# Kernel optimization log

Hardware: AMD Instinct MI355X
Metric: run time of the kernel (lower is better)

The kernel has to match this reference:

```python
import jax, jax.numpy as jnp
import numpy as np

R = 8            # ring rank
N = 4            # num cores
D_IN = 2048
D_OUT = 2048
LIN = [512, 512, 512, 512]   # local input dims (additive split)
LOUT = [512, 512, 512, 512]  # local output dims (additive split)


def setup_inputs() -> dict:
    key = jax.random.key(0)
    ks = jax.random.split(key, 6)
    inp = {"inputs": jax.random.normal(ks[0], (4, 1024, D_IN), dtype=jnp.float32)}
    for i in range(N):
        lf = LOUT[i] * LIN[i]
        std = np.sqrt(2.0 / (R + lf)).astype(np.float32)
        inp[f"core{i}"] = jax.random.normal(ks[1 + i], (R, lf, R), dtype=jnp.float32) * std
    inp["bias"] = jnp.zeros((D_OUT,), dtype=jnp.float32)
    return inp


def reference(inputs, core0, core1, core2, core3, bias):
    cores = [core0, core1, core2, core3]
    batch_shape = inputs.shape[:-1]
    x = inputs.reshape(-1, D_IN)                      # [B, D_IN]
    B = x.shape[0]

    # split input additively across cores
    offs = np.cumsum([0] + LIN)
    xs = [x[:, offs[i]:offs[i + 1]] for i in range(N)]  # each [B, d_in_i]
    Gs = [cores[i].reshape(R, LOUT[i], LIN[i], R) for i in range(N)]

    # environment messages: S_i[b,r,s] = sum_{o,x} G_i[r,o,x,s] * x_i[b,x]
    S = [jnp.einsum('roxs,bx->brs', Gs[i], xs[i]) for i in range(N)]

    eye = jnp.broadcast_to(jnp.eye(R, dtype=x.dtype), (B, R, R))
    # prefix P_i = S_0 ... S_{i-1}, suffix Q_i = S_{i+1} ... S_{N-1}
    P = [eye]
    for i in range(1, N):
        P.append(jnp.matmul(P[-1], S[i - 1]))
    Q = [eye]
    for i in range(N - 2, -1, -1):
        Q.append(jnp.matmul(S[i + 1], Q[-1]))
    Q = Q[::-1]

    outs = []
    for i in range(N):
        # Env_i[b,r,s] = sum_p Q_i[b,s,p] P_i[b,p,r]  (trace closure of the ring)
        env = jnp.einsum('bsp,bpr->brs', Q[i], P[i])
        # M_i[b,r,o,s] = sum_x G_i[r,o,x,s] x_i[b,x]
        M = jnp.einsum('roxs,bx->bros', Gs[i], xs[i])
        outs.append(jnp.einsum('brs,bros->bo', env, M))
    out = jnp.concatenate(outs, axis=-1) + bias       # [B, D_OUT]
    return out.reshape(batch_shape + (D_OUT,))
```

## Files before the change

kernel.cpp:

```cpp
#include <hip/hip_runtime.h>

#define B_TOT   4096
#define D_IN    2048
#define D_OUT   2048
#define NCHUNK  4
#define LIN     512
#define LOUT    512
#define RK      8
#define KXS     4096
#define CORE_R_STRIDE 2097152
#define CORE_O_STRIDE 4096

#define WS_XT    0
#define WS_GHAT  8388608
#define WS_S     (8388608 + 131072)
#define WS_ENVT  (8388608 + 131072 + 1048576)

typedef __attribute__((ext_vector_type(8))) __bf16 bf16x8;
typedef __attribute__((ext_vector_type(4))) float f32x4;
typedef __attribute__((ext_vector_type(4))) unsigned int u32x4;

__global__ __launch_bounds__(256) void k_transpose(const float* __restrict__ x,
                                                   float* __restrict__ xT) {
    __shared__ float tile[32][33];
    int b0 = blockIdx.x * 32;
    int c0 = blockIdx.y * 32;
    int tx = threadIdx.x;
    int ty = threadIdx.y;
#pragma unroll
    for (int j = 0; j < 4; ++j)
        tile[ty + j * 8][tx] = x[(size_t)(b0 + ty + j * 8) * D_IN + c0 + tx];
    __syncthreads();
#pragma unroll
    for (int j = 0; j < 4; ++j)
        xT[(size_t)(c0 + ty + j * 8) * B_TOT + b0 + tx] = tile[tx][ty + j * 8];
}

__global__ __launch_bounds__(256) void k_reduce_g(const float* __restrict__ g0,
                                                  const float* __restrict__ g1,
                                                  const float* __restrict__ g2,
                                                  const float* __restrict__ g3,
                                                  float* __restrict__ ghat) {
    int i = blockIdx.z;
    int r = blockIdx.y;
    int xs = blockIdx.x * 256 + threadIdx.x;
    const float* G = (i == 0) ? g0 : (i == 1) ? g1 : (i == 2) ? g2 : g3;
    const float* base = G + (size_t)r * CORE_R_STRIDE + xs;
    float acc = 0.f;
#pragma unroll 8
    for (int o = 0; o < LOUT; ++o) acc += base[(size_t)o * CORE_O_STRIDE];
    ghat[(size_t)i * 32768 + r * 4096 + xs] = acc;
}

__global__ __launch_bounds__(256) void k_s(const float* __restrict__ x,
                                           const float* __restrict__ ghat,
                                           float* __restrict__ S) {
    int i = blockIdx.y;
    int tid = threadIdx.x;
    int rs = tid & 63;
    int b = blockIdx.x * 4 + (tid >> 6);
    int r = rs >> 3, s = rs & 7;
    const float* gh = ghat + (size_t)i * 32768 + r * 4096 + s;
    const float* xr = x + (size_t)b * D_IN + i * LIN;
    float acc = 0.f;
#pragma unroll 8
    for (int xi = 0; xi < LIN; ++xi) acc = fmaf(gh[xi * 8], xr[xi], acc);
    S[(size_t)i * (B_TOT * 64) + b * 64 + rs] = acc;
}

__device__ __forceinline__ float mm8(float A, float B, int lane) {
    float c = 0.f;
#pragma unroll
    for (int p = 0; p < 8; ++p) {
        float a = __shfl(A, (lane & 56) | p, 64);
        float b = __shfl(B, (p << 3) | (lane & 7), 64);
        c = fmaf(a, b, c);
    }
    return c;
}
__device__ __forceinline__ float tr8(float E, int lane) {
    return __shfl(E, ((lane & 7) << 3) | (lane >> 3), 64);
}

__global__ __launch_bounds__(256) void k_env(const float* __restrict__ S,
                                             float* __restrict__ envT) {
    int tid = threadIdx.x;
    int lane = tid & 63;
    int b = blockIdx.x * 4 + (tid >> 6);
    float S0 = S[0 * (B_TOT * 64) + b * 64 + lane];
    float S1 = S[1 * (B_TOT * 64) + b * 64 + lane];
    float S2 = S[2 * (B_TOT * 64) + b * 64 + lane];
    float S3 = S[3 * (B_TOT * 64) + b * 64 + lane];

    float P1 = S0;
    float P2 = mm8(P1, S1, lane);
    float P3 = mm8(P2, S2, lane);
    float Q2 = S3;
    float Q1 = mm8(S2, Q2, lane);
    float Q0 = mm8(S1, Q1, lane);

    float e0 = tr8(Q0, lane);
    float e1 = tr8(mm8(Q1, P1, lane), lane);
    float e2 = tr8(mm8(Q2, P2, lane), lane);
    float e3 = tr8(P3, lane);

    envT[(size_t)(0 * 64 + lane) * B_TOT + b] = e0;
    envT[(size_t)(1 * 64 + lane) * B_TOT + b] = e1;
    envT[(size_t)(2 * 64 + lane) * B_TOT + b] = e2;
    envT[(size_t)(3 * 64 + lane) * B_TOT + b] = e3;
}

__device__ __forceinline__ uint2 split2(float a, float b) {
    unsigned int ua = __float_as_uint(a), ub = __float_as_uint(b);
    unsigned int h = (ub & 0xffff0000u) | (ua >> 16);
    float la = a - __uint_as_float(ua & 0xffff0000u);
    float lb = b - __uint_as_float(ub & 0xffff0000u);
    unsigned int l = (__float_as_uint(lb) & 0xffff0000u) | (__float_as_uint(la) >> 16);
    return make_uint2(h, l);
}

__global__ __launch_bounds__(256, 2) void k_gemm_mfma(const float* __restrict__ g0,
                                                      const float* __restrict__ g1,
                                                      const float* __restrict__ g2,
                                                      const float* __restrict__ g3,
                                                      const float* __restrict__ xT,
                                                      const float* __restrict__ envT,
                                                      const float* __restrict__ bias,
                                                      float* __restrict__ out) {
    int l = blockIdx.x;
    int c = (l & 7) | (((l >> 3) >> 5) << 3);
    int b_idx = (l >> 3) & 31;
    int i = c >> 2;
    int o0 = (c & 3) * 128;
    int b0 = b_idx * 128;

    const float* G = (i == 0) ? g0 : (i == 1) ? g1 : (i == 2) ? g2 : g3;
    const float* xTi = xT + (size_t)i * LIN * B_TOT;
    const float* eTi = envT + (size_t)i * 64 * B_TOT;

    __shared__ __align__(16) short Bhi[128 * 32];
    __shared__ __align__(16) short Blo[128 * 32];
    __shared__ float Xs[4][160];

    const int tid = threadIdx.x;
    const int lane = tid & 63;
    const int wave = tid >> 6;
    const int wm = (wave >> 1) * 64;
    const int wn = (wave & 1) * 64;
    const int l15 = lane & 15;
    const int quad = lane >> 4;

    f32x4 acc[4][4];
#pragma unroll
    for (int mf = 0; mf < 4; ++mf)
#pragma unroll
        for (int nf = 0; nf < 4; ++nf) acc[mf][nf] = (f32x4){0.f, 0.f, 0.f, 0.f};

    const int so = tid >> 1;
    const int sh = (tid & 1) * 16;
    const float* gbase = G + (size_t)(o0 + so) * CORE_O_STRIDE + sh;

    for (int r = 0; r < 8; ++r) {
        float e[4][8];
#pragma unroll
        for (int mf = 0; mf < 4; ++mf) {
            int m = b0 + wm + mf * 16 + l15;
#pragma unroll
            for (int s = 0; s < 8; ++s)
                e[mf][s] = eTi[(size_t)(r * 8 + s) * B_TOT + m];
        }
        const float* Gr = gbase + (size_t)r * CORE_R_STRIDE;

        for (int kk = 0; kk < 128; ++kk) {
            const int k0 = kk * 32;
            __syncthreads();
            if (tid < 128) {
                int xr = tid >> 5, bc = (tid & 31) * 4;
                *(float4*)&Xs[xr][bc] =
                    *(const float4*)&xTi[(size_t)(kk * 4 + xr) * B_TOT + b0 + bc];
            }
            {
                float4 f0 = *(const float4*)&Gr[k0 + 0];
                float4 f1 = *(const float4*)&Gr[k0 + 4];
                float4 f2 = *(const float4*)&Gr[k0 + 8];
                float4 f3 = *(const float4*)&Gr[k0 + 12];
                u32x4 H0, L0, H1, L1;
                uint2 p;
                p = split2(f0.x, f0.y); H0.x = p.x; L0.x = p.y;
                p = split2(f0.z, f0.w); H0.y = p.x; L0.y = p.y;
                p = split2(f1.x, f1.y); H0.z = p.x; L0.z = p.y;
                p = split2(f1.z, f1.w); H0.w = p.x; L0.w = p.y;
                p = split2(f2.x, f2.y); H1.x = p.x; L1.x = p.y;
                p = split2(f2.z, f2.w); H1.y = p.x; L1.y = p.y;
                p = split2(f3.x, f3.y); H1.z = p.x; L1.z = p.y;
                p = split2(f3.z, f3.w); H1.w = p.x; L1.w = p.y;
                *(u32x4*)&Bhi[so * 32 + sh] = H0;
                *(u32x4*)&Bhi[so * 32 + sh + 8] = H1;
                *(u32x4*)&Blo[so * 32 + sh] = L0;
                *(u32x4*)&Blo[so * 32 + sh + 8] = L1;
            }
            __syncthreads();

            bf16x8 bh[4], bl[4];
#pragma unroll
            for (int nf = 0; nf < 4; ++nf) {
                int n = wn + nf * 16 + l15;
                bh[nf] = *(const bf16x8*)&Bhi[n * 32 + quad * 8];
                bl[nf] = *(const bf16x8*)&Blo[n * 32 + quad * 8];
            }

#pragma unroll
            for (int mf = 0; mf < 4; ++mf) {
                float xv = Xs[quad][wm + mf * 16 + l15];
                u32x4 AH, AL;
                uint2 p;
                p = split2(e[mf][0] * xv, e[mf][1] * xv); AH.x = p.x; AL.x = p.y;
                p = split2(e[mf][2] * xv, e[mf][3] * xv); AH.y = p.x; AL.y = p.y;
                p = split2(e[mf][4] * xv, e[mf][5] * xv); AH.z = p.x; AL.z = p.y;
                p = split2(e[mf][6] * xv, e[mf][7] * xv); AH.w = p.x; AL.w = p.y;
                bf16x8 Ah = __builtin_bit_cast(bf16x8, AH);
                bf16x8 Al = __builtin_bit_cast(bf16x8, AL);
#pragma unroll
                for (int nf = 0; nf < 4; ++nf) {
                    acc[mf][nf] = __builtin_amdgcn_mfma_f32_16x16x32_bf16(Ah, bh[nf], acc[mf][nf], 0, 0, 0);
                    acc[mf][nf] = __builtin_amdgcn_mfma_f32_16x16x32_bf16(Ah, bl[nf], acc[mf][nf], 0, 0, 0);
                    acc[mf][nf] = __builtin_amdgcn_mfma_f32_16x16x32_bf16(Al, bh[nf], acc[mf][nf], 0, 0, 0);
                }
            }
        }
    }

#pragma unroll
    for (int nf = 0; nf < 4; ++nf) {
        int col = o0 + wn + nf * 16 + l15;
        float bv = bias[i * LOUT + col];
#pragma unroll
        for (int mf = 0; mf < 4; ++mf) {
#pragma unroll
            for (int reg = 0; reg < 4; ++reg) {
                int row = b0 + wm + mf * 16 + quad * 4 + reg;
                out[(size_t)row * D_OUT + i * LOUT + col] = acc[mf][nf][reg] + bv;
            }
        }
    }
}

extern "C" void kernel_launch(void* const* d_in, const int* in_sizes, int n_in,
                              void* d_out, int out_size, void* d_ws, size_t ws_size,
                              hipStream_t stream) {
    const float* x    = (const float*)d_in[0];
    const float* g0   = (const float*)d_in[1];
    const float* g1   = (const float*)d_in[2];
    const float* g2   = (const float*)d_in[3];
    const float* g3   = (const float*)d_in[4];
    const float* bias = (const float*)d_in[5];
    float* out = (float*)d_out;
    float* ws = (float*)d_ws;

    float* xT   = ws + WS_XT;
    float* ghat = ws + WS_GHAT;
    float* S    = ws + WS_S;
    float* envT = ws + WS_ENVT;

    k_transpose<<<dim3(128, 64), dim3(32, 8), 0, stream>>>(x, xT);
    k_reduce_g<<<dim3(16, 8, 4), 256, 0, stream>>>(g0, g1, g2, g3, ghat);
    k_s<<<dim3(1024, 4), 256, 0, stream>>>(x, ghat, S);
    k_env<<<1024, 256, 0, stream>>>(S, envT);
    k_gemm_mfma<<<512, 256, 0, stream>>>(g0, g1, g2, g3, xT, envT, bias, out);
}
```

Baseline: 2.333 ms.

## Pre-split core weights into bf16 hi/lo planes and stream via global_load_lds

Adds a pass that splits each fp32 core weight into bf16 high and low planes in workspace once per call. A new GEMM kernel then streams those planes directly into LDS with double-buffered global_load_lds, instead of splitting weights inside the main loop. This is meant to take conversion ALU work and register staging out of the hot loop. In exchange it adds a full extra read of the 256MB of weights plus about 256MB of writes and reads of the split planes. It only runs when the workspace is large enough, and falls back to the old kernel otherwise.

```diff
diff --git a/kernel.cpp b/kernel.cpp
--- a/kernel.cpp
+++ b/kernel.cpp
@@ -1,4 +1,5 @@
 #include <hip/hip_runtime.h>
+#include <stdint.h>
 
 #define B_TOT   4096
 #define D_IN    2048
@@ -7,7 +8,6 @@
 #define LIN     512
 #define LOUT    512
 #define RK      8
-#define KXS     4096
 #define CORE_R_STRIDE 2097152
 #define CORE_O_STRIDE 4096
 
@@ -15,6 +15,10 @@
 #define WS_GHAT  8388608
 #define WS_S     (8388608 + 131072)
 #define WS_ENVT  (8388608 + 131072 + 1048576)
+#define WS_GSPL  (8388608 + 131072 + 1048576 + 1048576)
+#define GSPL_PLANE 67108864ull
+#define GSPL_CHUNK 16777216ull
+#define WS_NEED_BYTES 310902784ull
 
 typedef __attribute__((ext_vector_type(8))) __bf16 bf16x8;
 typedef __attribute__((ext_vector_type(4))) float f32x4;
@@ -117,6 +121,159 @@
     float lb = b - __uint_as_float(ub & 0xffff0000u);
     unsigned int l = (__float_as_uint(lb) & 0xffff0000u) | (__float_as_uint(la) >> 16);
     return make_uint2(h, l);
+}
+
+__global__ __launch_bounds__(256) void k_split_g(const float* __restrict__ g0,
+                                                 const float* __restrict__ g1,
+                                                 const float* __restrict__ g2,
+                                                 const float* __restrict__ g3,
+                                                 short* __restrict__ hi,
+                                                 short* __restrict__ lo) {
+    size_t e8 = ((size_t)blockIdx.x * 256 + threadIdx.x) * 8;
+    int i = (int)(e8 >> 24);
+    const float* G = (i == 0) ? g0 : (i == 1) ? g1 : (i == 2) ? g2 : g3;
+    size_t off = e8 & (GSPL_CHUNK - 1);
+    float4 f0 = *(const float4*)(G + off);
+    float4 f1 = *(const float4*)(G + off + 4);
+    u32x4 H, L;
+    uint2 p;
+    p = split2(f0.x, f0.y); H.x = p.x; L.x = p.y;
+    p = split2(f0.z, f0.w); H.y = p.x; L.y = p.y;
+    p = split2(f1.x, f1.y); H.z = p.x; L.z = p.y;
+    p = split2(f1.z, f1.w); H.w = p.x; L.w = p.y;
+    *(u32x4*)(hi + e8) = H;
+    *(u32x4*)(lo + e8) = L;
+}
+
+__device__ __forceinline__ void gld16(const void* g, void* l) {
+    __builtin_amdgcn_global_load_lds(
+        (const __attribute__((address_space(1))) void*)g,
+        (__attribute__((address_space(3))) void*)l, 16, 0, 0);
+}
+
+__global__ __launch_bounds__(256, 2) void k_gemm2(const short* __restrict__ ghi,
+                                                  const short* __restrict__ glo,
+                                                  const float* __restrict__ xT,
+                                                  const float* __restrict__ envT,
+                                                  const float* __restrict__ bias,
+                                                  float* __restrict__ out) {
+    int l = blockIdx.x;
+    int c = (l & 7) | ((l >> 8) << 3);
+    int b_idx = (l >> 3) & 31;
+    int i = c >> 2;
+    int o0 = (c & 3) * 128;
+    int b0 = b_idx * 128;
+
+    const short* Hi = ghi + (size_t)i * GSPL_CHUNK;
+    const short* Lo = glo + (size_t)i * GSPL_CHUNK;
+    const float* xTi = xT + (size_t)i * LIN * B_TOT;
+    const float* eTi = envT + (size_t)i * 64 * B_TOT;
+
+    __shared__ __align__(16) short Bhi[2][4096];
+    __shared__ __align__(16) short Blo[2][4096];
+
+    const int tid = threadIdx.x;
+    const int lane = tid & 63;
+    const int wave = tid >> 6;
+    const int wm = (wave >> 1) * 64;
+    const int wn = (wave & 1) * 64;
+    const int l15 = lane & 15;
+    const int quad = lane >> 4;
+    const int lq = lane >> 2;
+    const int ls = lane & 3;
+    const int w32 = wave * 32;
+
+    f32x4 acc[4][4];
+#pragma unroll
+    for (int mf = 0; mf < 4; ++mf)
+#pragma unroll
+        for (int nf = 0; nf < 4; ++nf) acc[mf][nf] = (f32x4){0.f, 0.f, 0.f, 0.f};
+
+    auto STAGE = [&](int tn, int pb) {
+#pragma unroll
+        for (int j = 0; j < 2; ++j) {
+            int row = w32 + j * 16 + lq;
+            int sl = ls ^ ((row >> 1) & 3);
+            size_t soff = ((size_t)((tn >> 7) * 512 + o0 + row) << 12)
+                        + (size_t)(tn & 127) * 32 + sl * 8;
+            int doff = wave * 1024 + j * 512;
+            gld16(Hi + soff, &Bhi[pb][doff]);
+            gld16(Lo + soff, &Blo[pb][doff]);
+        }
+    };
+
+    float xc[4], xn[4];
+#pragma unroll
+    for (int mf = 0; mf < 4; ++mf)
+        xc[mf] = xTi[(size_t)quad * B_TOT + b0 + wm + mf * 16 + l15];
+
+    STAGE(0, 0);
+    __syncthreads();
+
+    int t = 0;
+    for (int r = 0; r < 8; ++r) {
+        float e[4][8];
+#pragma unroll
+        for (int mf = 0; mf < 4; ++mf) {
+            int m = b0 + wm + mf * 16 + l15;
+#pragma unroll
+            for (int s = 0; s < 8; ++s)
+                e[mf][s] = eTi[(size_t)(r * 8 + s) * B_TOT + m];
+        }
+        for (int kk = 0; kk < 128; ++kk, ++t) {
+            const int p = t & 1;
+            if (t + 1 < 1024) STAGE(t + 1, p ^ 1);
+#pragma unroll
+            for (int mf = 0; mf < 4; ++mf)
+                xn[mf] = xTi[(size_t)(((kk + 1) & 127) * 4 + quad) * B_TOT
+                             + b0 + wm + mf * 16 + l15];
+
+            bf16x8 bh[4], bl[4];
+#pragma unroll
+            for (int nf = 0; nf < 4; ++nf) {
+                int n = wn + nf * 16 + l15;
+                int sl = quad ^ ((n >> 1) & 3);
+                bh[nf] = *(const bf16x8*)&Bhi[p][n * 32 + sl * 8];
+                bl[nf] = *(const bf16x8*)&Blo[p][n * 32 + sl * 8];
+            }
+
+#pragma unroll
+            for (int mf = 0; mf < 4; ++mf) {
+                float xv = xc[mf];
+                u32x4 AH, AL;
+                uint2 pr;
+                pr = split2(e[mf][0] * xv, e[mf][1] * xv); AH.x = pr.x; AL.x = pr.y;
+                pr = split2(e[mf][2] * xv, e[mf][3] * xv); AH.y = pr.x; AL.y = pr.y;
+                pr = split2(e[mf][4] * xv, e[mf][5] * xv); AH.z = pr.x; AL.z = pr.y;
+                pr = split2(e[mf][6] * xv, e[mf][7] * xv); AH.w = pr.x; AL.w = pr.y;
+                bf16x8 Ah = __builtin_bit_cast(bf16x8, AH);
+                bf16x8 Al = __builtin_bit_cast(bf16x8, AL);
+#pragma unroll
+                for (int nf = 0; nf < 4; ++nf) {
+                    acc[mf][nf] = __builtin_amdgcn_mfma_f32_16x16x32_bf16(Ah, bh[nf], acc[mf][nf], 0, 0, 0);
+                    acc[mf][nf] = __builtin_amdgcn_mfma_f32_16x16x32_bf16(Ah, bl[nf], acc[mf][nf], 0, 0, 0);
+                    acc[mf][nf] = __builtin_amdgcn_mfma_f32_16x16x32_bf16(Al, bh[nf], acc[mf][nf], 0, 0, 0);
+                }
+            }
+            __syncthreads();
+#pragma unroll
+            for (int mf = 0; mf < 4; ++mf) xc[mf] = xn[mf];
+        }
+    }
+
+#pragma unroll
+    for (int nf = 0; nf < 4; ++nf) {
+        int col = o0 + wn + nf * 16 + l15;
+        float bv = bias[i * LOUT + col];
+#pragma unroll
+        for (int mf = 0; mf < 4; ++mf) {
+#pragma unroll
+            for (int reg = 0; reg < 4; ++reg) {
+                int row = b0 + wm + mf * 16 + quad * 4 + reg;
+                out[(size_t)row * D_OUT + i * LOUT + col] = acc[mf][nf][reg] + bv;
+            }
+        }
+    }
 }
 
 __global__ __launch_bounds__(256, 2) void k_gemm_mfma(const float* __restrict__ g0,
@@ -266,5 +423,13 @@
     k_reduce_g<<<dim3(16, 8, 4), 256, 0, stream>>>(g0, g1, g2, g3, ghat);
     k_s<<<dim3(1024, 4), 256, 0, stream>>>(x, ghat, S);
     k_env<<<1024, 256, 0, stream>>>(S, envT);
-    k_gemm_mfma<<<512, 256, 0, stream>>>(g0, g1, g2, g3, xT, envT, bias, out);
-}
+
+    if (ws_size >= (size_t)WS_NEED_BYTES) {
+        short* ghi = (short*)(ws + WS_GSPL);
+        short* glo = ghi + GSPL_PLANE;
+        k_split_g<<<32768, 256, 0, stream>>>(g0, g1, g2, g3, ghi, glo);
+        k_gemm2<<<512, 256, 0, stream>>>(ghi, glo, xT, envT, bias, out);
+    } else {
+        k_gemm_mfma<<<512, 256, 0, stream>>>(g0, g1, g2, g3, xT, envT, bias, out);
+    }
+}
```

New measurement: 2.328 ms. No clear change (-0.2%).

## Double-buffer core tiles in LDS and prefetch next tile during MFMA

Applied to the files above, without the earlier changes.

The main GEMM kernel now double-buffers the split bf16 hi/lo core tiles in shared memory. It loads the next tile's global data into registers before running the MFMA work on the current buffer, then splits and stores it into the other buffer, so only one barrier is needed per k-step instead of two. The x values are read straight from global memory into registers, one step ahead, instead of being staged through shared memory. LDS rows are padded (stride 40 shorts) to reduce bank conflicts. In exchange it uses more registers and doubles the LDS footprint, which could lower occupancy.

```diff
diff --git a/kernel.cpp b/kernel.cpp
--- a/kernel.cpp
+++ b/kernel.cpp
@@ -1,4 +1,5 @@
 #include <hip/hip_runtime.h>
+#include <stdint.h>
 
 #define B_TOT   4096
 #define D_IN    2048
@@ -7,7 +8,6 @@
 #define LIN     512
 #define LOUT    512
 #define RK      8
-#define KXS     4096
 #define CORE_R_STRIDE 2097152
 #define CORE_O_STRIDE 4096
 
@@ -119,7 +119,7 @@
     return make_uint2(h, l);
 }
 
-__global__ __launch_bounds__(256, 2) void k_gemm_mfma(const float* __restrict__ g0,
+__global__ __launch_bounds__(256, 2) void k_gemm_pipe(const float* __restrict__ g0,
                                                       const float* __restrict__ g1,
                                                       const float* __restrict__ g2,
                                                       const float* __restrict__ g3,
@@ -138,9 +138,8 @@
     const float* xTi = xT + (size_t)i * LIN * B_TOT;
     const float* eTi = envT + (size_t)i * 64 * B_TOT;
 
-    __shared__ __align__(16) short Bhi[128 * 32];
-    __shared__ __align__(16) short Blo[128 * 32];
-    __shared__ float Xs[4][160];
+    __shared__ __align__(16) short Bhi[2][5120];
+    __shared__ __align__(16) short Blo[2][5120];
 
     const int tid = threadIdx.x;
     const int lane = tid & 63;
@@ -150,16 +149,53 @@
     const int l15 = lane & 15;
     const int quad = lane >> 4;
 
-    f32x4 acc[4][4];
-#pragma unroll
-    for (int mf = 0; mf < 4; ++mf)
-#pragma unroll
-        for (int nf = 0; nf < 4; ++nf) acc[mf][nf] = (f32x4){0.f, 0.f, 0.f, 0.f};
-
     const int so = tid >> 1;
     const int sh = (tid & 1) * 16;
-    const float* gbase = G + (size_t)(o0 + so) * CORE_O_STRIDE + sh;
-
+    const int s0 = (tid & 1) * 2;
+    const float* gsrc = G + (size_t)(o0 + so) * CORE_O_STRIDE + sh;
+
+    f32x4 acc[4][4];
+#pragma unroll
+    for (int mf = 0; mf < 4; ++mf)
+#pragma unroll
+        for (int nf = 0; nf < 4; ++nf) acc[mf][nf] = (f32x4){0.f, 0.f, 0.f, 0.f};
+
+    float4 f0, f1, f2, f3;
+
+    auto LOADG = [&](int tn) {
+        const float* p = gsrc + (size_t)(tn >> 7) * CORE_R_STRIDE + (tn & 127) * 32;
+        f0 = *(const float4*)(p);
+        f1 = *(const float4*)(p + 4);
+        f2 = *(const float4*)(p + 8);
+        f3 = *(const float4*)(p + 12);
+    };
+    auto STORE = [&](int pb) {
+        u32x4 H0, L0, H1, L1;
+        uint2 q;
+        q = split2(f0.x, f0.y); H0.x = q.x; L0.x = q.y;
+        q = split2(f0.z, f0.w); H0.y = q.x; L0.y = q.y;
+        q = split2(f1.x, f1.y); H0.z = q.x; L0.z = q.y;
+        q = split2(f1.z, f1.w); H0.w = q.x; L0.w = q.y;
+        q = split2(f2.x, f2.y); H1.x = q.x; L1.x = q.y;
+        q = split2(f2.z, f2.w); H1.y = q.x; L1.y = q.y;
+        q = split2(f3.x, f3.y); H1.z = q.x; L1.z = q.y;
+        q = split2(f3.z, f3.w); H1.w = q.x; L1.w = q.y;
+        *(u32x4*)&Bhi[pb][(so * 5 + s0) * 8]     = H0;
+        *(u32x4*)&Bhi[pb][(so * 5 + s0 + 1) * 8] = H1;
+        *(u32x4*)&Blo[pb][(so * 5 + s0) * 8]     = L0;
+        *(u32x4*)&Blo[pb][(so * 5 + s0 + 1) * 8] = L1;
+    };
+
+    float xc[4], xn[4];
+#pragma unroll
+    for (int mf = 0; mf < 4; ++mf)
+        xc[mf] = xTi[(size_t)quad * B_TOT + b0 + wm + mf * 16 + l15];
+
+    LOADG(0);
+    STORE(0);
+    __syncthreads();
+
+    int t = 0;
     for (int r = 0; r < 8; ++r) {
         float e[4][8];
 #pragma unroll
@@ -169,55 +205,32 @@
             for (int s = 0; s < 8; ++s)
                 e[mf][s] = eTi[(size_t)(r * 8 + s) * B_TOT + m];
         }
-        const float* Gr = gbase + (size_t)r * CORE_R_STRIDE;
-
-        for (int kk = 0; kk < 128; ++kk) {
-            const int k0 = kk * 32;
-            __syncthreads();
-            if (tid < 128) {
-                int xr = tid >> 5, bc = (tid & 31) * 4;
-                *(float4*)&Xs[xr][bc] =
-                    *(const float4*)&xTi[(size_t)(kk * 4 + xr) * B_TOT + b0 + bc];
-            }
-            {
-                float4 f0 = *(const float4*)&Gr[k0 + 0];
-                float4 f1 = *(const float4*)&Gr[k0 + 4];
-                float4 f2 = *(const float4*)&Gr[k0 + 8];
-                float4 f3 = *(const float4*)&Gr[k0 + 12];
-                u32x4 H0, L0, H1, L1;
-                uint2 p;
-                p = split2(f0.x, f0.y); H0.x = p.x; L0.x = p.y;
-                p = split2(f0.z, f0.w); H0.y = p.x; L0.y = p.y;
-                p = split2(f1.x, f1.y); H0.z = p.x; L0.z = p.y;
-                p = split2(f1.z, f1.w); H0.w = p.x; L0.w = p.y;
-                p = split2(f2.x, f2.y); H1.x = p.x; L1.x = p.y;
-                p = split2(f2.z, f2.w); H1.y = p.x; L1.y = p.y;
-                p = split2(f3.x, f3.y); H1.z = p.x; L1.z = p.y;
-                p = split2(f3.z, f3.w); H1.w = p.x; L1.w = p.y;
-                *(u32x4*)&Bhi[so * 32 + sh] = H0;
-                *(u32x4*)&Bhi[so * 32 + sh + 8] = H1;
-                *(u32x4*)&Blo[so * 32 + sh] = L0;
-                *(u32x4*)&Blo[so * 32 + sh + 8] = L1;
-            }
-            __syncthreads();
+        for (int kk = 0; kk < 128; ++kk, ++t) {
+            const int p = t & 1;
+            const bool more = (t + 1 < 1024);
+            if (more) LOADG(t + 1);
+#pragma unroll
+            for (int mf = 0; mf < 4; ++mf)
+                xn[mf] = xTi[(size_t)(((kk + 1) & 127) * 4 + quad) * B_TOT
+                             + b0 + wm + mf * 16 + l15];
 
             bf16x8 bh[4], bl[4];
 #pragma unroll
             for (int nf = 0; nf < 4; ++nf) {
                 int n = wn + nf * 16 + l15;
-                bh[nf] = *(const bf16x8*)&Bhi[n * 32 + quad * 8];
-                bl[nf] = *(const bf16x8*)&Blo[n * 32 + quad * 8];
+                bh[nf] = *(const bf16x8*)&Bhi[p][(n * 5 + quad) * 8];
+                bl[nf] = *(const bf16x8*)&Blo[p][(n * 5 + quad) * 8];
             }
 
 #pragma unroll
             for (int mf = 0; mf < 4; ++mf) {
-                float xv = Xs[quad][wm + mf * 16 + l15];
+                float xv = xc[mf];
                 u32x4 AH, AL;
-                uint2 p;
-                p = split2(e[mf][0] * xv, e[mf][1] * xv); AH.x = p.x; AL.x = p.y;
-                p = split2(e[mf][2] * xv, e[mf][3] * xv); AH.y = p.x; AL.y = p.y;
-                p = split2(e[mf][4] * xv, e[mf][5] * xv); AH.z = p.x; AL.z = p.y;
-                p = split2(e[mf][6] * xv, e[mf][7] * xv); AH.w = p.x; AL.w = p.y;
+                uint2 pr;
+                pr = split2(e[mf][0] * xv, e[mf][1] * xv); AH.x = pr.x; AL.x = pr.y;
+                pr = split2(e[mf][2] * xv, e[mf][3] * xv); AH.y = pr.x; AL.y = pr.y;
+                pr = split2(e[mf][4] * xv, e[mf][5] * xv); AH.z = pr.x; AL.z = pr.y;
+                pr = split2(e[mf][6] * xv, e[mf][7] * xv); AH.w = pr.x; AL.w = pr.y;
                 bf16x8 Ah = __builtin_bit_cast(bf16x8, AH);
                 bf16x8 Al = __builtin_bit_cast(bf16x8, AL);
 #pragma unroll
@@ -227,6 +240,11 @@
                     acc[mf][nf] = __builtin_amdgcn_mfma_f32_16x16x32_bf16(Al, bh[nf], acc[mf][nf], 0, 0, 0);
                 }
             }
+
+            if (more) STORE(p ^ 1);
+            __syncthreads();
+#pragma unroll
+            for (int mf = 0; mf < 4; ++mf) xc[mf] = xn[mf];
         }
     }
 
@@ -266,5 +284,5 @@
     k_reduce_g<<<dim3(16, 8, 4), 256, 0, stream>>>(g0, g1, g2, g3, ghat);
     k_s<<<dim3(1024, 4), 256, 0, stream>>>(x, ghat, S);
     k_env<<<1024, 256, 0, stream>>>(S, envT);
-    k_gemm_mfma<<<512, 256, 0, stream>>>(g0, g1, g2, g3, xT, envT, bias, out);
-}
+    k_gemm_pipe<<<512, 256, 0, stream>>>(g0, g1, g2, g3, xT, envT, bias, out);
+}
```

Measured after the change: 2.331 ms. About the same (-0.1%).
